# Performance work log

Hardware: AMD Instinct MI355X
Metric: run time of the kernel (lower is better)

Reference implementation:

```python
import jax, jax.numpy as jnp
import numpy as np

N, E, F_IN = 50000, 1_600_000, 256
HID, HEADS, NCLS = 8, 8, 16  # conv1: 8 heads x 8 dims (concat=64); conv2: 1 head -> 16 classes


def setup_inputs() -> dict:
    key = jax.random.key(0)
    ks = jax.random.split(key, 11)
    x = jax.random.normal(ks[0], (N, F_IN), dtype=jnp.float32)
    edge_index = jax.random.randint(ks[1], (2, E), 0, N, dtype=jnp.int32)
    s1 = 1.0 / np.sqrt(F_IN)
    W1 = jax.random.normal(ks[2], (F_IN, HEADS * HID), jnp.float32) * s1
    a_src1 = jax.random.normal(ks[3], (HEADS, HID), jnp.float32) * 0.1
    a_dst1 = jax.random.normal(ks[4], (HEADS, HID), jnp.float32) * 0.1
    b1 = jnp.zeros((HEADS * HID,), jnp.float32)
    s2 = 1.0 / np.sqrt(HEADS * HID)
    W2 = jax.random.normal(ks[5], (HEADS * HID, NCLS), jnp.float32) * s2
    a_src2 = jax.random.normal(ks[6], (1, NCLS), jnp.float32) * 0.1
    a_dst2 = jax.random.normal(ks[7], (1, NCLS), jnp.float32) * 0.1
    b2 = jnp.zeros((NCLS,), jnp.float32)
    return {"x": x, "edge_index": edge_index, "W1": W1, "a_src1": a_src1,
            "a_dst1": a_dst1, "b1": b1, "W2": W2, "a_src2": a_src2,
            "a_dst2": a_dst2, "b2": b2}


def _gat_conv(x, W, a_src, a_dst, bias, src, dst, n, heads, ch, concat):
    # per-head linear transform: [n, heads, ch]
    h = (x @ W).reshape(n, heads, ch)
    # additive attention logits per node, per head
    al_s = jnp.einsum('nhc,hc->nh', h, a_src)
    al_d = jnp.einsum('nhc,hc->nh', h, a_dst)
    e = jax.nn.leaky_relu(al_s[src] + al_d[dst], 0.2)  # [E_tot, heads]
    # segment softmax grouped by destination node (self-loops guarantee non-empty segments)
    m = jax.ops.segment_max(e, dst, num_segments=n)
    ex = jnp.exp(e - m[dst])
    den = jax.ops.segment_sum(ex, dst, num_segments=n)
    alpha = ex / den[dst]  # [E_tot, heads]
    # scatter-aggregate weighted neighbor features
    out = jax.ops.segment_sum(h[src] * alpha[:, :, None], dst, num_segments=n)
    out = out.reshape(n, heads * ch) if concat else out.mean(axis=1)
    return out + bias


def reference(x, edge_index, W1, a_src1, a_dst1, b1, W2, a_src2, a_dst2, b2):
    # add self-loops (PyG GATConv default)
    loops = jnp.arange(N, dtype=edge_index.dtype)
    src = jnp.concatenate([edge_index[0], loops])
    dst = jnp.concatenate([edge_index[1], loops])
    h = _gat_conv(x, W1, a_src1, a_dst1, b1, src, dst, N, HEADS, HID, True)
    h = jax.nn.elu(h)
    out = _gat_conv(h, W2, a_src2, a_dst2, b2, src, dst, N, 1, NCLS, False)
    return jax.nn.log_softmax(out, axis=1)
```

## Files before the change

### kernel.cpp

```cpp
#include <hip/hip_runtime.h>
#include <hip/hip_fp16.h>

#define NN   50000
#define FIN  256
#define C1   64
#define NH   8
#define NC   16
#define NE   1600000
#define NTOT (NE + NN)

#define CH   256
#define EPC  ((NTOT + CH - 1) / CH)
#define NCB  196
#define GB1  ((NN + 63) / 64)

typedef _Float16 half8 __attribute__((ext_vector_type(8)));
typedef _Float16 half4 __attribute__((ext_vector_type(4)));
typedef float f32x4 __attribute__((ext_vector_type(4)));

#define OFF_H1H   0
#define OFF_G1H   1600000
#define OFF_STAGE 3200000
#define OFF_H2H   3200000
#define OFF_ALS2  3600000
#define OFF_ALD2  3650000
#define OFF_ALS1  6400000
#define OFF_ALD1  6800000
#define OFF_HM    7200000
#define OFF_BASEK 7251000
#define OFF_BBASE 7302000
#define OFF_OFFS  7302400
#define OFF_SRC   7352500

__global__ __launch_bounds__(256) void k_g1rh(const float* __restrict__ x,
                                              const float* __restrict__ W1,
                                              const float* __restrict__ as1,
                                              const float* __restrict__ ad1,
                                              __half* __restrict__ h1h,
                                              float* __restrict__ als,
                                              float* __restrict__ ald,
                                              const int* __restrict__ ei,
                                              int* __restrict__ H) {
    __shared__ _Float16 wsT[64][264];
    __shared__ _Float16 xs[64][40];
    __shared__ int lh[NCB];
    const int tid = threadIdx.x;

    if (blockIdx.x >= GB1) {
        int k = blockIdx.x - GB1;
        for (int i = tid; i < NCB; i += 256) lh[i] = 0;
        __syncthreads();
        int e0 = k * EPC, e1 = min(e0 + EPC, NTOT);
        for (int e = e0 + tid; e < e1; e += 256) {
            int d = (e < NE) ? ei[NE + e] : (e - NE);
            atomicAdd(&lh[d >> 8], 1);
        }
        __syncthreads();
        for (int i = tid; i < NCB; i += 256) H[k * NCB + i] = lh[i];
        return;
    }

    const int r0 = blockIdx.x * 64;
    {
        int c = tid & 63, kb = tid >> 6;
        #pragma unroll
        for (int j = 0; j < 8; ++j) {
            int k8 = kb + 4 * j;
            half8 hv;
            #pragma unroll
            for (int u = 0; u < 8; ++u)
                hv[u] = (_Float16)W1[(size_t)(k8 * 8 + u) * C1 + c];
            *(half8*)(&wsT[c][k8 * 8]) = hv;
        }
    }

    const int lane = tid & 63;
    const int wv   = tid >> 6;
    const int colb = lane & 15;
    const int rgrp = lane >> 4;
    f32x4 acc[4] = {};
    const int srow = tid >> 2;
    const int sq   = tid & 3;
    for (int k0 = 0; k0 < FIN; k0 += 32) {
        __syncthreads();
        {
            int grow = r0 + srow;
            float4 v0 = make_float4(0.f,0.f,0.f,0.f), v1 = v0;
            if (grow < NN) {
                const float4* xp = (const float4*)(&x[(size_t)grow * FIN + k0 + sq * 8]);
                v0 = xp[0]; v1 = xp[1];
            }
            half8 hv;
            hv[0]=(_Float16)v0.x; hv[1]=(_Float16)v0.y; hv[2]=(_Float16)v0.z; hv[3]=(_Float16)v0.w;
            hv[4]=(_Float16)v1.x; hv[5]=(_Float16)v1.y; hv[6]=(_Float16)v1.z; hv[7]=(_Float16)v1.w;
            *(half8*)(&xs[srow][sq * 8]) = hv;
        }
        __syncthreads();
        half8 a = *(half8*)(&xs[wv * 16 + colb][rgrp * 8]);
        #pragma unroll
        for (int ct = 0; ct < 4; ++ct) {
            half8 b = *(half8*)(&wsT[ct * 16 + colb][k0 + rgrp * 8]);
            acc[ct] = __builtin_amdgcn_mfma_f32_16x16x32_f16(a, b, acc[ct], 0, 0, 0);
        }
    }

    float a_s[4], a_d[4];
    #pragma unroll
    for (int ct = 0; ct < 4; ++ct) { a_s[ct] = as1[ct * 16 + colb]; a_d[ct] = ad1[ct * 16 + colb]; }
    #pragma unroll
    for (int j = 0; j < 4; ++j) {
        int row = r0 + wv * 16 + rgrp * 4 + j;
        bool rv = row < NN;
        #pragma unroll
        for (int ct = 0; ct < 4; ++ct) {
            if (rv) h1h[(size_t)row * C1 + ct * 16 + colb] = __float2half(acc[ct][j]);
            float p = acc[ct][j] * a_s[ct];
            p += __shfl_xor(p, 1); p += __shfl_xor(p, 2); p += __shfl_xor(p, 4);
            float q = acc[ct][j] * a_d[ct];
            q += __shfl_xor(q, 1); q += __shfl_xor(q, 2); q += __shfl_xor(q, 4);
            if (rv && (lane & 7) == 0) {
                int head = ct * 2 + (colb >> 3);
                als[row * NH + head] = p;
                ald[row * NH + head] = q;
            }
        }
    }
}

__global__ __launch_bounds__(256) void k_rsA(const int* __restrict__ H,
                                             int* __restrict__ basek,
                                             int* __restrict__ btot) {
    __shared__ int sc[CH];
    int b = blockIdx.x, t = threadIdx.x;
    int v = H[t * NCB + b];
    sc[t] = v;
    __syncthreads();
    for (int s = 1; s < CH; s <<= 1) {
        int u = (t >= s) ? sc[t - s] : 0;
        __syncthreads();
        sc[t] += u;
        __syncthreads();
    }
    basek[b * CH + t] = sc[t] - v;
    if (t == CH - 1) btot[b] = sc[t];
}

__global__ __launch_bounds__(256) void k_rsB(const int* __restrict__ btot,
                                             int* __restrict__ bbase,
                                             int* __restrict__ offs) {
    __shared__ int sc[256];
    int t = threadIdx.x;
    int v = (t < NCB) ? btot[t] : 0;
    sc[t] = v;
    __syncthreads();
    for (int s = 1; s < 256; s <<= 1) {
        int u = (t >= s) ? sc[t - s] : 0;
        __syncthreads();
        sc[t] += u;
        __syncthreads();
    }
    if (t < NCB) bbase[t] = sc[t] - v;
    if (t == NCB - 1) bbase[NCB] = sc[t];
    if (t == 0) offs[NN] = NTOT;
}

__global__ __launch_bounds__(256) void k_rscatter(const int* __restrict__ ei,
                                                  const int* __restrict__ basek,
                                                  const int* __restrict__ bbase,
                                                  int* __restrict__ stage) {
    __shared__ int lcur[NCB];
    int k = blockIdx.x;
    for (int i = threadIdx.x; i < NCB; i += 256)
        lcur[i] = bbase[i] + basek[i * CH + k];
    __syncthreads();
    int e0 = k * EPC, e1 = min(e0 + EPC, NTOT);
    for (int e = e0 + threadIdx.x; e < e1; e += 256) {
        int s, d;
        if (e < NE) { s = ei[e]; d = ei[NE + e]; }
        else        { s = e - NE; d = s; }
        int pos = atomicAdd(&lcur[d >> 8], 1);
        stage[pos] = (s << 8) | (d & 255);
    }
}

__global__ __launch_bounds__(256) void k_fsort(const int* __restrict__ stage,
                                               const int* __restrict__ bbase,
                                               int* __restrict__ offs,
                                               int* __restrict__ ssrc) {
    __shared__ int lc[256];
    __shared__ int ls[256];
    __shared__ int lcur[256];
    int b = blockIdx.x, t = threadIdx.x;
    int base = bbase[b];
    int n = bbase[b + 1] - base;
    lc[t] = 0;
    __syncthreads();
    const int* sp = &stage[base];
    for (int i = t; i < n; i += 256) atomicAdd(&lc[sp[i] & 255], 1);
    __syncthreads();
    int v = lc[t];
    ls[t] = v;
    __syncthreads();
    for (int s = 1; s < 256; s <<= 1) {
        int u = (t >= s) ? ls[t - s] : 0;
        __syncthreads();
        ls[t] += u;
        __syncthreads();
    }
    int excl = ls[t] - v;
    int d = b * 256 + t;
    if (d < NN) offs[d] = base + excl;
    lcur[t] = base + excl;
    __syncthreads();
    for (int i = t; i < n; i += 256) {
        int u = sp[i];
        int pos = atomicAdd(&lcur[u & 255], 1);
        ssrc[pos] = u >> 8;
    }
}

__global__ __launch_bounds__(256) void k_agg1(const int* __restrict__ offs,
                                              const int* __restrict__ src,
                                              const __half* __restrict__ h1h,
                                              const float* __restrict__ als,
                                              const float* __restrict__ ald,
                                              const float* __restrict__ b1,
                                              _Float16* __restrict__ g1h) {
    int d = blockIdx.x * 4 + (threadIdx.x >> 6);
    if (d >= NN) return;
    const int l  = threadIdx.x & 63;
    const int q  = l >> 4, lc = l & 15;
    const int hg = lc >> 1;
    const int sub = l >> 3, hw = l & 7;
    const int lane_a = (q << 3) | hg;
    const int lane_b = lane_a + 32;
    int beg = offs[d], end = offs[d + 1];
    float aldv = ald[d * NH + hw];
    f32x4 acc = {0.f, 0.f, 0.f, 0.f};
    float den = 0.f;

    for (int r = beg; r < end; r += 16) {
        int e0 = r + sub, e1 = e0 + 8;
        bool v0 = e0 < end, v1 = e1 < end;
        int s0 = src[v0 ? e0 : end - 1];
        int s1 = src[v1 ? e1 : end - 1];
        float lg0 = als[s0 * NH + hw] + aldv;
        float lg1 = als[s1 * NH + hw] + aldv;
        lg0 = lg0 > 0.f ? lg0 : 0.2f * lg0;
        lg1 = lg1 > 0.f ? lg1 : 0.2f * lg1;
        float w0 = v0 ? __expf(lg0) : 0.f;
        float w1 = v1 ? __expf(lg1) : 0.f;
        #pragma unroll
        for (int i = 0; i < 4; ++i) {
            int srcl = (i & 1) ? lane_b : lane_a;
            int sv   = __shfl((i < 2) ? s0 : s1, srcl);
            float wvv= __shfl((i < 2) ? w0 : w1, srcl);
            half4 hv = *(const half4*)(&h1h[(size_t)sv * C1 + 4 * lc]);
            acc[0] += wvv * (float)hv[0];
            acc[1] += wvv * (float)hv[1];
            acc[2] += wvv * (float)hv[2];
            acc[3] += wvv * (float)hv[3];
            den += wvv;
        }
    }
    #pragma unroll
    for (int k = 0; k < 4; ++k) {
        acc[k] += __shfl_xor(acc[k], 16);
        acc[k] += __shfl_xor(acc[k], 32);
    }
    den += __shfl_xor(den, 16);
    den += __shfl_xor(den, 32);
    if (q == 0) {
        half4 gv;
        #pragma unroll
        for (int k = 0; k < 4; ++k) {
            float o = acc[k] / den + b1[4 * lc + k];
            o = o > 0.f ? o : (__expf(o) - 1.f);
            gv[k] = (_Float16)o;
        }
        *(half4*)(&g1h[(size_t)d * C1 + 4 * lc]) = gv;
    }
}

__global__ __launch_bounds__(256) void k_gemm2(const _Float16* __restrict__ g1h,
                                               const float* __restrict__ W2,
                                               const float* __restrict__ as2,
                                               const float* __restrict__ ad2,
                                               _Float16* __restrict__ h2h,
                                               float* __restrict__ als2,
                                               float* __restrict__ ald2) {
    __shared__ float w2s[C1][17];
    __shared__ _Float16 hact[16][C1 + 8];
    int tid = threadIdx.x;
    for (int i = tid; i < C1 * NC; i += 256) w2s[i >> 4][i & 15] = W2[i];
    int ln = tid >> 4, j = tid & 15;
    int n = blockIdx.x * 16 + ln;
    if (n < NN)
        *(half4*)(&hact[ln][j * 4]) = *(const half4*)(&g1h[(size_t)n * C1 + j * 4]);
    __syncthreads();
    if (n >= NN) return;
    float sum = 0.f;
    #pragma unroll
    for (int c = 0; c < C1; ++c) sum += (float)hact[ln][c] * w2s[c][j];
    h2h[(size_t)n * NC + j] = (_Float16)sum;
    float ps = sum * as2[j], pd = sum * ad2[j];
    #pragma unroll
    for (int w = 1; w < 16; w <<= 1) {
        ps += __shfl_xor(ps, w);
        pd += __shfl_xor(pd, w);
    }
    if (j == 0) { als2[n] = ps; ald2[n] = pd; }
}

__global__ __launch_bounds__(256) void k_agg2(const int* __restrict__ offs,
                                              const int* __restrict__ src,
                                              const _Float16* __restrict__ h2h,
                                              const float* __restrict__ als2,
                                              const float* __restrict__ ald2,
                                              const float* __restrict__ b2,
                                              float* __restrict__ out) {
    int d = blockIdx.x * 16 + (threadIdx.x >> 4);
    if (d >= NN) return;
    int c = threadIdx.x & 15;
    int beg = offs[d], end = offs[d + 1];
    float aldv = ald2[d];
    float acc = 0.f, den = 0.f;
    for (int r = beg; r < end; r += 4) {
        int e1 = r + 1, e2 = r + 2, e3 = r + 3;
        bool v1 = e1 < end, v2 = e2 < end, v3 = e3 < end;
        int s0 = src[r];
        int s1 = src[v1 ? e1 : end - 1];
        int s2 = src[v2 ? e2 : end - 1];
        int s3 = src[v3 ? e3 : end - 1];
        float l0 = als2[s0] + aldv;
        float l1 = als2[s1] + aldv;
        float l2 = als2[s2] + aldv;
        float l3 = als2[s3] + aldv;
        l0 = l0 > 0.f ? l0 : 0.2f * l0;
        l1 = l1 > 0.f ? l1 : 0.2f * l1;
        l2 = l2 > 0.f ? l2 : 0.2f * l2;
        l3 = l3 > 0.f ? l3 : 0.2f * l3;
        float w0 = __expf(l0);
        float w1 = v1 ? __expf(l1) : 0.f;
        float w2 = v2 ? __expf(l2) : 0.f;
        float w3 = v3 ? __expf(l3) : 0.f;
        float f0 = (float)h2h[(size_t)s0 * NC + c];
        float f1 = (float)h2h[(size_t)s1 * NC + c];
        float f2 = (float)h2h[(size_t)s2 * NC + c];
        float f3 = (float)h2h[(size_t)s3 * NC + c];
        acc += w0 * f0 + w1 * f1 + w2 * f2 + w3 * f3;
        den += w0 + w1 + w2 + w3;
    }
    float o = acc / den + b2[c];
    float m = o;
    #pragma unroll
    for (int w = 1; w < 16; w <<= 1) m = fmaxf(m, __shfl_xor(m, w));
    float ex = __expf(o - m);
    float sm = ex;
    #pragma unroll
    for (int w = 1; w < 16; w <<= 1) sm += __shfl_xor(sm, w);
    out[(size_t)d * NC + c] = o - m - __logf(sm);
}

extern "C" void kernel_launch(void* const* d_in, const int* in_sizes, int n_in,
                              void* d_out, int out_size, void* d_ws, size_t ws_size,
                              hipStream_t stream) {
    const float* x   = (const float*)d_in[0];
    const int*   ei  = (const int*)  d_in[1];
    const float* W1  = (const float*)d_in[2];
    const float* as1 = (const float*)d_in[3];
    const float* ad1 = (const float*)d_in[4];
    const float* b1  = (const float*)d_in[5];
    const float* W2  = (const float*)d_in[6];
    const float* as2 = (const float*)d_in[7];
    const float* ad2 = (const float*)d_in[8];
    const float* b2  = (const float*)d_in[9];
    float* ws  = (float*)d_ws;
    float* out = (float*)d_out;

    __half*    h1h  = (__half*)(ws + OFF_H1H);
    _Float16*  g1h  = (_Float16*)(ws + OFF_G1H);
    _Float16*  h2h  = (_Float16*)(ws + OFF_H2H);
    float* als1 = ws + OFF_ALS1;
    float* ald1 = ws + OFF_ALD1;
    float* als2 = ws + OFF_ALS2;
    float* ald2 = ws + OFF_ALD2;
    int* H      = (int*)(ws + OFF_HM);
    int* basek  = (int*)(ws + OFF_BASEK);
    int* bbase  = (int*)(ws + OFF_BBASE);
    int* offs   = (int*)(ws + OFF_OFFS);
    int* ssrc   = (int*)(ws + OFF_SRC);
    int* stage  = (int*)(ws + OFF_STAGE);

    k_g1rh    <<<GB1 + CH,       256, 0, stream>>>(x, W1, as1, ad1, h1h, als1, ald1, ei, H);
    k_rsA     <<<NCB,            256, 0, stream>>>(H, basek, bbase + NCB + 2 );
    k_rsB     <<<1,              256, 0, stream>>>(bbase + NCB + 2, bbase, offs);
    k_rscatter<<<CH,             256, 0, stream>>>(ei, basek, bbase, stage);
    k_fsort   <<<NCB,            256, 0, stream>>>(stage, bbase, offs, ssrc);
    k_agg1    <<<(NN + 3) / 4,   256, 0, stream>>>(offs, ssrc, h1h, als1, ald1, b1, g1h);
    k_gemm2   <<<(NN + 15) / 16, 256, 0, stream>>>(g1h, W2, as2, ad2, h2h, als2, ald2);
    k_agg2    <<<(NN + 15) / 16, 256, 0, stream>>>(offs, ssrc, h2h, als2, ald2, b2, out);
}
```

Baseline: 138.0 us.

## Pre-transpose W1, narrow sort buckets, prefetch indices in aggregation kernels

Adds a small kernel that converts and transposes W1 to fp16 once, so each GEMM block can load its weight tile with vector loads instead of strided scalar loads. The coarse destination buckets shrink from 256 to 128 nodes (392 buckets), which gives the fine sort more blocks and less per-block work, and the block-total scan grows to 512 threads to match. agg1 software-prefetches the next edge indices, uses 32-bit byte offsets and computes the denominator once per head instead of inside the inner loop. agg2 unrolls to 8 edges and batches its gathers. These touch several independent stages, and the extra launch adds fixed overhead.

```diff
diff --git a/kernel.cpp b/kernel.cpp
--- a/kernel.cpp
+++ b/kernel.cpp
@@ -11,7 +11,7 @@
 
 #define CH   256
 #define EPC  ((NTOT + CH - 1) / CH)
-#define NCB  196
+#define NCB  392
 #define GB1  ((NN + 63) / 64)
 
 typedef _Float16 half8 __attribute__((ext_vector_type(8)));
@@ -27,13 +27,21 @@
 #define OFF_ALS1  6400000
 #define OFF_ALD1  6800000
 #define OFF_HM    7200000
-#define OFF_BASEK 7251000
-#define OFF_BBASE 7302000
-#define OFF_OFFS  7302400
-#define OFF_SRC   7352500
+#define OFF_BASEK 7300352
+#define OFF_BBASE 7400704
+#define OFF_OFFS  7401600
+#define OFF_SRC   7451700
+#define OFF_W1T   9101700
+
+__global__ __launch_bounds__(256) void k_wcvt(const float* __restrict__ W1,
+                                              _Float16* __restrict__ w1t) {
+    int t = blockIdx.x * 256 + threadIdx.x;
+    int c = t >> 8, k = t & 255;
+    w1t[t] = (_Float16)W1[k * C1 + c];
+}
 
 __global__ __launch_bounds__(256) void k_g1rh(const float* __restrict__ x,
-                                              const float* __restrict__ W1,
+                                              const _Float16* __restrict__ w1t,
                                               const float* __restrict__ as1,
                                               const float* __restrict__ ad1,
                                               __half* __restrict__ h1h,
@@ -43,17 +51,17 @@
                                               int* __restrict__ H) {
     __shared__ _Float16 wsT[64][264];
     __shared__ _Float16 xs[64][40];
-    __shared__ int lh[NCB];
     const int tid = threadIdx.x;
 
     if (blockIdx.x >= GB1) {
+        int* lh = (int*)xs;
         int k = blockIdx.x - GB1;
         for (int i = tid; i < NCB; i += 256) lh[i] = 0;
         __syncthreads();
         int e0 = k * EPC, e1 = min(e0 + EPC, NTOT);
         for (int e = e0 + tid; e < e1; e += 256) {
             int d = (e < NE) ? ei[NE + e] : (e - NE);
-            atomicAdd(&lh[d >> 8], 1);
+            atomicAdd(&lh[d >> 7], 1);
         }
         __syncthreads();
         for (int i = tid; i < NCB; i += 256) H[k * NCB + i] = lh[i];
@@ -61,17 +69,11 @@
     }
 
     const int r0 = blockIdx.x * 64;
-    {
-        int c = tid & 63, kb = tid >> 6;
-        #pragma unroll
-        for (int j = 0; j < 8; ++j) {
-            int k8 = kb + 4 * j;
-            half8 hv;
-            #pragma unroll
-            for (int u = 0; u < 8; ++u)
-                hv[u] = (_Float16)W1[(size_t)(k8 * 8 + u) * C1 + c];
-            *(half8*)(&wsT[c][k8 * 8]) = hv;
-        }
+    #pragma unroll
+    for (int j = 0; j < 8; ++j) {
+        int idx = tid * 8 + j * 2048;
+        int c = idx >> 8, ko = idx & 255;
+        *(half8*)(&wsT[c][ko]) = *(const half8*)(&w1t[idx]);
     }
 
     const int lane = tid & 63;
@@ -145,15 +147,15 @@
     if (t == CH - 1) btot[b] = sc[t];
 }
 
-__global__ __launch_bounds__(256) void k_rsB(const int* __restrict__ btot,
+__global__ __launch_bounds__(512) void k_rsB(const int* __restrict__ btot,
                                              int* __restrict__ bbase,
                                              int* __restrict__ offs) {
-    __shared__ int sc[256];
+    __shared__ int sc[512];
     int t = threadIdx.x;
     int v = (t < NCB) ? btot[t] : 0;
     sc[t] = v;
     __syncthreads();
-    for (int s = 1; s < 256; s <<= 1) {
+    for (int s = 1; s < 512; s <<= 1) {
         int u = (t >= s) ? sc[t - s] : 0;
         __syncthreads();
         sc[t] += u;
@@ -178,8 +180,8 @@
         int s, d;
         if (e < NE) { s = ei[e]; d = ei[NE + e]; }
         else        { s = e - NE; d = s; }
-        int pos = atomicAdd(&lcur[d >> 8], 1);
-        stage[pos] = (s << 8) | (d & 255);
+        int pos = atomicAdd(&lcur[d >> 7], 1);
+        stage[pos] = (s << 7) | (d & 127);
     }
 }
 
@@ -187,35 +189,37 @@
                                                const int* __restrict__ bbase,
                                                int* __restrict__ offs,
                                                int* __restrict__ ssrc) {
-    __shared__ int lc[256];
-    __shared__ int ls[256];
-    __shared__ int lcur[256];
+    __shared__ int lc[128];
+    __shared__ int ls[128];
+    __shared__ int lcur[128];
     int b = blockIdx.x, t = threadIdx.x;
     int base = bbase[b];
     int n = bbase[b + 1] - base;
-    lc[t] = 0;
+    if (t < 128) lc[t] = 0;
     __syncthreads();
     const int* sp = &stage[base];
-    for (int i = t; i < n; i += 256) atomicAdd(&lc[sp[i] & 255], 1);
-    __syncthreads();
-    int v = lc[t];
-    ls[t] = v;
-    __syncthreads();
-    for (int s = 1; s < 256; s <<= 1) {
-        int u = (t >= s) ? ls[t - s] : 0;
-        __syncthreads();
-        ls[t] += u;
-        __syncthreads();
-    }
-    int excl = ls[t] - v;
-    int d = b * 256 + t;
-    if (d < NN) offs[d] = base + excl;
-    lcur[t] = base + excl;
+    for (int i = t; i < n; i += 256) atomicAdd(&lc[sp[i] & 127], 1);
+    __syncthreads();
+    int v = (t < 128) ? lc[t] : 0;
+    if (t < 128) ls[t] = v;
+    __syncthreads();
+    for (int s = 1; s < 128; s <<= 1) {
+        int u = (t >= s && t < 128) ? ls[t - s] : 0;
+        __syncthreads();
+        if (t < 128) ls[t] += u;
+        __syncthreads();
+    }
+    if (t < 128) {
+        int excl = ls[t] - v;
+        int d = b * 128 + t;
+        if (d < NN) offs[d] = base + excl;
+        lcur[t] = base + excl;
+    }
     __syncthreads();
     for (int i = t; i < n; i += 256) {
         int u = sp[i];
-        int pos = atomicAdd(&lcur[u & 255], 1);
-        ssrc[pos] = u >> 8;
+        int pos = atomicAdd(&lcur[u & 127], 1);
+        ssrc[pos] = u >> 7;
     }
 }
 
@@ -234,42 +238,57 @@
     const int sub = l >> 3, hw = l & 7;
     const int lane_a = (q << 3) | hg;
     const int lane_b = lane_a + 32;
+    const unsigned coff = (unsigned)lc * 8u;
+    const unsigned hoff = (unsigned)hw * 4u;
+    const char* h1b = (const char*)h1h;
+    const char* alb = (const char*)als;
     int beg = offs[d], end = offs[d + 1];
     float aldv = ald[d * NH + hw];
     f32x4 acc = {0.f, 0.f, 0.f, 0.f};
-    float den = 0.f;
-
-    for (int r = beg; r < end; r += 16) {
-        int e0 = r + sub, e1 = e0 + 8;
-        bool v0 = e0 < end, v1 = e1 < end;
-        int s0 = src[v0 ? e0 : end - 1];
-        int s1 = src[v1 ? e1 : end - 1];
-        float lg0 = als[s0 * NH + hw] + aldv;
-        float lg1 = als[s1 * NH + hw] + aldv;
+    float wsum = 0.f;
+
+    int r = beg;
+    int e0 = r + sub, e1 = e0 + 8;
+    int s0 = src[e0 < end ? e0 : end - 1];
+    int s1 = src[e1 < end ? e1 : end - 1];
+    while (r < end) {
+        bool v0 = (r + sub) < end, v1 = (r + 8 + sub) < end;
+        float lg0 = *(const float*)(alb + ((unsigned)s0 * 32u + hoff)) + aldv;
+        float lg1 = *(const float*)(alb + ((unsigned)s1 * 32u + hoff)) + aldv;
         lg0 = lg0 > 0.f ? lg0 : 0.2f * lg0;
         lg1 = lg1 > 0.f ? lg1 : 0.2f * lg1;
         float w0 = v0 ? __expf(lg0) : 0.f;
         float w1 = v1 ? __expf(lg1) : 0.f;
+        wsum += w0 + w1;
+        int rn = r + 16;
+        int s0n = s0, s1n = s1;
+        if (rn < end) {
+            int f0 = rn + sub, f1 = f0 + 8;
+            s0n = src[f0 < end ? f0 : end - 1];
+            s1n = src[f1 < end ? f1 : end - 1];
+        }
         #pragma unroll
         for (int i = 0; i < 4; ++i) {
             int srcl = (i & 1) ? lane_b : lane_a;
             int sv   = __shfl((i < 2) ? s0 : s1, srcl);
-            float wvv= __shfl((i < 2) ? w0 : w1, srcl);
-            half4 hv = *(const half4*)(&h1h[(size_t)sv * C1 + 4 * lc]);
-            acc[0] += wvv * (float)hv[0];
-            acc[1] += wvv * (float)hv[1];
-            acc[2] += wvv * (float)hv[2];
-            acc[3] += wvv * (float)hv[3];
-            den += wvv;
-        }
+            float wv = __shfl((i < 2) ? w0 : w1, srcl);
+            half4 hv = *(const half4*)(h1b + ((unsigned)sv * 128u + coff));
+            acc[0] += wv * (float)hv[0];
+            acc[1] += wv * (float)hv[1];
+            acc[2] += wv * (float)hv[2];
+            acc[3] += wv * (float)hv[3];
+        }
+        s0 = s0n; s1 = s1n; r = rn;
     }
     #pragma unroll
     for (int k = 0; k < 4; ++k) {
         acc[k] += __shfl_xor(acc[k], 16);
         acc[k] += __shfl_xor(acc[k], 32);
     }
-    den += __shfl_xor(den, 16);
-    den += __shfl_xor(den, 32);
+    wsum += __shfl_xor(wsum, 8);
+    wsum += __shfl_xor(wsum, 16);
+    wsum += __shfl_xor(wsum, 32);
+    float den = __shfl(wsum, hg);
     if (q == 0) {
         half4 gv;
         #pragma unroll
@@ -322,34 +341,32 @@
     int d = blockIdx.x * 16 + (threadIdx.x >> 4);
     if (d >= NN) return;
     int c = threadIdx.x & 15;
+    const unsigned coff = (unsigned)c * 2u;
+    const char* h2b = (const char*)h2h;
+    const char* alb = (const char*)als2;
     int beg = offs[d], end = offs[d + 1];
     float aldv = ald2[d];
     float acc = 0.f, den = 0.f;
-    for (int r = beg; r < end; r += 4) {
-        int e1 = r + 1, e2 = r + 2, e3 = r + 3;
-        bool v1 = e1 < end, v2 = e2 < end, v3 = e3 < end;
-        int s0 = src[r];
-        int s1 = src[v1 ? e1 : end - 1];
-        int s2 = src[v2 ? e2 : end - 1];
-        int s3 = src[v3 ? e3 : end - 1];
-        float l0 = als2[s0] + aldv;
-        float l1 = als2[s1] + aldv;
-        float l2 = als2[s2] + aldv;
-        float l3 = als2[s3] + aldv;
-        l0 = l0 > 0.f ? l0 : 0.2f * l0;
-        l1 = l1 > 0.f ? l1 : 0.2f * l1;
-        l2 = l2 > 0.f ? l2 : 0.2f * l2;
-        l3 = l3 > 0.f ? l3 : 0.2f * l3;
-        float w0 = __expf(l0);
-        float w1 = v1 ? __expf(l1) : 0.f;
-        float w2 = v2 ? __expf(l2) : 0.f;
-        float w3 = v3 ? __expf(l3) : 0.f;
-        float f0 = (float)h2h[(size_t)s0 * NC + c];
-        float f1 = (float)h2h[(size_t)s1 * NC + c];
-        float f2 = (float)h2h[(size_t)s2 * NC + c];
-        float f3 = (float)h2h[(size_t)s3 * NC + c];
-        acc += w0 * f0 + w1 * f1 + w2 * f2 + w3 * f3;
-        den += w0 + w1 + w2 + w3;
+    for (int r = beg; r < end; r += 8) {
+        int ss[8];
+        float ww[8];
+        #pragma unroll
+        for (int i = 0; i < 8; ++i) {
+            int e = r + i;
+            ss[i] = src[e < end ? e : end - 1];
+        }
+        #pragma unroll
+        for (int i = 0; i < 8; ++i) {
+            float lg = *(const float*)(alb + (unsigned)ss[i] * 4u) + aldv;
+            lg = lg > 0.f ? lg : 0.2f * lg;
+            ww[i] = (r + i) < end ? __expf(lg) : 0.f;
+        }
+        #pragma unroll
+        for (int i = 0; i < 8; ++i) {
+            float hv = (float)*(const _Float16*)(h2b + ((unsigned)ss[i] * 32u + coff));
+            acc += ww[i] * hv;
+            den += ww[i];
+        }
     }
     float o = acc / den + b2[c];
     float m = o;
@@ -381,6 +398,7 @@
     __half*    h1h  = (__half*)(ws + OFF_H1H);
     _Float16*  g1h  = (_Float16*)(ws + OFF_G1H);
     _Float16*  h2h  = (_Float16*)(ws + OFF_H2H);
+    _Float16*  w1t  = (_Float16*)(ws + OFF_W1T);
     float* als1 = ws + OFF_ALS1;
     float* ald1 = ws + OFF_ALD1;
     float* als2 = ws + OFF_ALS2;
@@ -388,13 +406,15 @@
     int* H      = (int*)(ws + OFF_HM);
     int* basek  = (int*)(ws + OFF_BASEK);
     int* bbase  = (int*)(ws + OFF_BBASE);
+    int* btot   = (int*)(ws + OFF_BBASE) + 400;
     int* offs   = (int*)(ws + OFF_OFFS);
     int* ssrc   = (int*)(ws + OFF_SRC);
     int* stage  = (int*)(ws + OFF_STAGE);
 
-    k_g1rh    <<<GB1 + CH,       256, 0, stream>>>(x, W1, as1, ad1, h1h, als1, ald1, ei, H);
-    k_rsA     <<<NCB,            256, 0, stream>>>(H, basek, bbase + NCB + 2 );
-    k_rsB     <<<1,              256, 0, stream>>>(bbase + NCB + 2, bbase, offs);
+    k_wcvt    <<<64,             256, 0, stream>>>(W1, w1t);
+    k_g1rh    <<<GB1 + CH,       256, 0, stream>>>(x, w1t, as1, ad1, h1h, als1, ald1, ei, H);
+    k_rsA     <<<NCB,            256, 0, stream>>>(H, basek, btot);
+    k_rsB     <<<1,              512, 0, stream>>>(btot, bbase, offs);
     k_rscatter<<<CH,             256, 0, stream>>>(ei, basek, bbase, stage);
     k_fsort   <<<NCB,            256, 0, stream>>>(stage, bbase, offs, ssrc);
     k_agg1    <<<(NN + 3) / 4,   256, 0, stream>>>(offs, ssrc, h1h, als1, ald1, b1, g1h);
```

Result: no change. 137.8 us (-0.1%).
